# Performance work log

Hardware: AMD Instinct MI355X
Metric: run time of the kernel (lower is better)

The kernel has to match this reference:

```python
import math
import jax, jax.numpy as jnp
import numpy as np

PHI = (1.0 + math.sqrt(5.0)) / 2.0
LUT_SIZE = 4096
_angles = np.arange(LUT_SIZE, dtype=np.float64) * (2.0 * math.pi / LUT_SIZE)
SIN_TABLE = jnp.asarray(np.sin(_angles), dtype=jnp.float32)
COS_TABLE = jnp.asarray(np.cos(_angles), dtype=jnp.float32)


def lut_sin_cos(theta):
    # LUT lookup with linear interpolation over a 4096-entry table on [0, 2pi)
    pos = theta * (LUT_SIZE / (2.0 * math.pi))
    i0f = jnp.floor(pos)
    frac = pos - i0f
    i0 = jnp.mod(i0f.astype(jnp.int32), LUT_SIZE)
    i1 = jnp.mod(i0 + 1, LUT_SIZE)
    sin_v = SIN_TABLE[i0] * (1.0 - frac) + SIN_TABLE[i1] * frac
    cos_v = COS_TABLE[i0] * (1.0 - frac) + COS_TABLE[i1] * frac
    return sin_v, cos_v


def setup_inputs() -> dict:
    key = jax.random.key(0)
    ks = jax.random.split(key, 8)
    B, D = 32768, 1024
    return {
        "x_real": jax.random.normal(ks[0], (B, D), jnp.float32),
        "x_imag": jax.random.normal(ks[1], (B, D), jnp.float32),
        "t": jax.random.uniform(ks[2], (B,), jnp.float32),
        "memory_real": jax.random.normal(ks[3], (B, D), jnp.float32),
        "memory_imag": jax.random.normal(ks[4], (B, D), jnp.float32),
        "w_query": jax.random.normal(ks[5], (D,), jnp.float32) * 0.02,
        "b_query": jnp.zeros((D,), jnp.float32),
        "w_osc": jax.random.normal(ks[6], (D,), jnp.float32) * 0.02,
        "b_osc": jnp.zeros((D,), jnp.float32),
    }


def reference(x_real, x_imag, t, memory_real, memory_imag, w_query, b_query, w_osc, b_osc):
    d_model = x_real.shape[-1]
    scale = math.sqrt(d_model)
    k = 1.0

    t_phi = t[:, None] * PHI                       # [B, 1]

    # query oscillator
    wl_query = 1.0 + jnp.abs(w_query)
    theta_query = x_real / wl_query + b_query      # [B, D]
    sin_q, cos_q = lut_sin_cos(theta_query)
    query_real, query_imag = cos_q, sin_q

    # memory interference (memory is detached state)
    mem_r = jax.lax.stop_gradient(memory_real)
    mem_i = jax.lax.stop_gradient(memory_imag)
    interference_real = jnp.sum(query_real * mem_r + query_imag * mem_i, axis=-1)
    interference_imag = jnp.sum(query_real * mem_i - query_imag * mem_r, axis=-1)
    interference_mag = jnp.sqrt(interference_real ** 2 + interference_imag ** 2)

    # alpha (exponential mode)
    interference_norm = jax.nn.sigmoid(interference_mag / scale - 2.0)
    x_inv = 1.0 - interference_norm
    alpha = jnp.exp(-k * x_inv)
    alpha_exp = alpha[:, None]

    # blend with memory
    blended_real = alpha_exp * x_real + (1.0 - alpha_exp) * mem_r
    blended_imag = alpha_exp * x_imag + (1.0 - alpha_exp) * mem_i

    # evolve oscillator
    wl_osc = 1.0 + jnp.abs(w_osc)
    theta_osc_real = blended_real / wl_osc + b_osc + t_phi
    theta_osc_imag = blended_imag / wl_osc + b_osc + t_phi
    sin_or, cos_or = lut_sin_cos(theta_osc_real)
    sin_oi, cos_oi = lut_sin_cos(theta_osc_imag)
    evolved_real = cos_or * cos_oi - sin_or * sin_oi
    evolved_imag = cos_or * sin_oi + sin_or * cos_oi

    return evolved_real, evolved_imag, alpha
```

## Files before the change

### kernel.cpp

```cpp
#include <hip/hip_runtime.h>
#include <math.h>

static constexpr float PHI_F = 1.61803398874989484820f;

union F4 { float4 v; float f[4]; };

__global__ __launch_bounds__(256) void liquid_echo_kernel(
    const float* __restrict__ x_real,
    const float* __restrict__ x_imag,
    const float* __restrict__ t,
    const float* __restrict__ mem_r,
    const float* __restrict__ mem_i,
    const float* __restrict__ w_query,
    const float* __restrict__ b_query,
    const float* __restrict__ w_osc,
    const float* __restrict__ b_osc,
    float* __restrict__ out_real,
    float* __restrict__ out_imag,
    float* __restrict__ out_alpha,
    int D)
{
    const int row = blockIdx.x;
    const int tid = threadIdx.x;
    const int d0  = tid << 2;
    const size_t base = (size_t)row * (size_t)D + (size_t)d0;

    F4 xr, xi, mr, mi, wq, bq, wo, bo;
    xr.v = *(const float4*)(x_real + base);
    xi.v = *(const float4*)(x_imag + base);
    mr.v = *(const float4*)(mem_r + base);
    mi.v = *(const float4*)(mem_i + base);
    wq.v = *(const float4*)(w_query + d0);
    bq.v = *(const float4*)(b_query + d0);
    wo.v = *(const float4*)(w_osc + d0);
    bo.v = *(const float4*)(b_osc + d0);

    float accr = 0.f, acci = 0.f;
#pragma unroll
    for (int j = 0; j < 4; ++j) {
        float inv = __builtin_amdgcn_rcpf(1.0f + fabsf(wq.f[j]));
        float th  = fmaf(xr.f[j], inv, bq.f[j]);
        float s, c;
        __sincosf(th, &s, &c);
        accr = fmaf(c, mr.f[j], fmaf(s, mi.f[j], accr));
        acci = fmaf(c, mi.f[j], fmaf(-s, mr.f[j], acci));
    }

#pragma unroll
    for (int off = 32; off > 0; off >>= 1) {
        accr += __shfl_down(accr, off, 64);
        acci += __shfl_down(acci, off, 64);
    }
    __shared__ float sred[8];
    const int wave = tid >> 6;
    const int lane = tid & 63;
    if (lane == 0) { sred[wave] = accr; sred[wave + 4] = acci; }
    __syncthreads();
    const float ir = (sred[0] + sred[1]) + (sred[2] + sred[3]);
    const float ii = (sred[4] + sred[5]) + (sred[6] + sred[7]);

    const float mag   = sqrtf(fmaf(ir, ir, ii * ii));
    const float z     = fmaf(mag, 1.0f / 32.0f, -2.0f);
    const float norm  = __builtin_amdgcn_rcpf(1.0f + __expf(-z));
    const float alpha = __expf(norm - 1.0f);
    const float beta  = 1.0f - alpha;
    const float tphi2 = 2.0f * PHI_F * t[row];

    F4 er, ei;
#pragma unroll
    for (int j = 0; j < 4; ++j) {
        float br  = fmaf(alpha, xr.f[j], beta * mr.f[j]);
        float bi  = fmaf(alpha, xi.f[j], beta * mi.f[j]);
        float inv = __builtin_amdgcn_rcpf(1.0f + fabsf(wo.f[j]));
        float ths = fmaf(br + bi, inv, fmaf(2.0f, bo.f[j], tphi2));
        float s, c;
        __sincosf(ths, &s, &c);
        er.f[j] = c;
        ei.f[j] = s;
    }
    *(float4*)(out_real + base) = er.v;
    *(float4*)(out_imag + base) = ei.v;
    if (tid == 0) out_alpha[row] = alpha;
}

extern "C" void kernel_launch(void* const* d_in, const int* in_sizes, int n_in,
                              void* d_out, int out_size, void* d_ws, size_t ws_size,
                              hipStream_t stream) {
    const float* x_real = (const float*)d_in[0];
    const float* x_imag = (const float*)d_in[1];
    const float* t      = (const float*)d_in[2];
    const float* mem_r  = (const float*)d_in[3];
    const float* mem_i  = (const float*)d_in[4];
    const float* w_q    = (const float*)d_in[5];
    const float* b_q    = (const float*)d_in[6];
    const float* w_o    = (const float*)d_in[7];
    const float* b_o    = (const float*)d_in[8];

    const int B = in_sizes[2];
    const int D = in_sizes[5];

    float* out       = (float*)d_out;
    float* out_real  = out;
    float* out_imag  = out + (size_t)B * (size_t)D;
    float* out_alpha = out + 2ull * (size_t)B * (size_t)D;

    liquid_echo_kernel<<<B, 256, 0, stream>>>(
        x_real, x_imag, t, mem_r, mem_i, w_q, b_q, w_o, b_o,
        out_real, out_imag, out_alpha, D);
}
```

Measured before the change: 147.4 us.

## Map one row per wavefront to remove cross-wave shared-memory reduction

Each 64-lane wavefront now processes a whole 1024-element row, with each lane handling 16 elements, so the dot-product reduction is done purely with xor shuffles and no LDS or block barrier. The grid shrinks by four and the weight loads are split, with the oscillator weights loaded after the first phase. This trades the synchronisation cost for much higher register pressure per thread, which may reduce occupancy. It also hardcodes D=1024.

```diff
diff --git a/kernel.cpp b/kernel.cpp
--- a/kernel.cpp
+++ b/kernel.cpp
@@ -5,7 +5,7 @@
 
 union F4 { float4 v; float f[4]; };
 
-__global__ __launch_bounds__(256) void liquid_echo_kernel(
+__global__ __launch_bounds__(256, 4) void liquid_echo_kernel(
     const float* __restrict__ x_real,
     const float* __restrict__ x_imag,
     const float* __restrict__ t,
@@ -17,70 +17,87 @@
     const float* __restrict__ b_osc,
     float* __restrict__ out_real,
     float* __restrict__ out_imag,
-    float* __restrict__ out_alpha,
-    int D)
+    float* __restrict__ out_alpha)
 {
-    const int row = blockIdx.x;
-    const int tid = threadIdx.x;
-    const int d0  = tid << 2;
-    const size_t base = (size_t)row * (size_t)D + (size_t)d0;
+    const int lane = threadIdx.x & 63;
+    const int wave = threadIdx.x >> 6;
+    const int row  = (blockIdx.x << 2) + wave;
+    const size_t rbase = (size_t)row << 10;
 
-    F4 xr, xi, mr, mi, wq, bq, wo, bo;
-    xr.v = *(const float4*)(x_real + base);
-    xi.v = *(const float4*)(x_imag + base);
-    mr.v = *(const float4*)(mem_r + base);
-    mi.v = *(const float4*)(mem_i + base);
-    wq.v = *(const float4*)(w_query + d0);
-    bq.v = *(const float4*)(b_query + d0);
-    wo.v = *(const float4*)(w_osc + d0);
-    bo.v = *(const float4*)(b_osc + d0);
+    const float trow = t[row];
+
+    F4 xr[4], xi[4], mr[4], mi[4];
+#pragma unroll
+    for (int j = 0; j < 4; ++j) {
+        const size_t off = rbase + (size_t)(((j << 6) + lane) << 2);
+        xr[j].v = *(const float4*)(x_real + off);
+        xi[j].v = *(const float4*)(x_imag + off);
+        mr[j].v = *(const float4*)(mem_r + off);
+        mi[j].v = *(const float4*)(mem_i + off);
+    }
+    F4 wq[4], bq[4];
+#pragma unroll
+    for (int j = 0; j < 4; ++j) {
+        const int woff = ((j << 6) + lane) << 2;
+        wq[j].v = *(const float4*)(w_query + woff);
+        bq[j].v = *(const float4*)(b_query + woff);
+    }
 
     float accr = 0.f, acci = 0.f;
 #pragma unroll
     for (int j = 0; j < 4; ++j) {
-        float inv = __builtin_amdgcn_rcpf(1.0f + fabsf(wq.f[j]));
-        float th  = fmaf(xr.f[j], inv, bq.f[j]);
-        float s, c;
-        __sincosf(th, &s, &c);
-        accr = fmaf(c, mr.f[j], fmaf(s, mi.f[j], accr));
-        acci = fmaf(c, mi.f[j], fmaf(-s, mr.f[j], acci));
+#pragma unroll
+        for (int k = 0; k < 4; ++k) {
+            float inv = __builtin_amdgcn_rcpf(1.0f + fabsf(wq[j].f[k]));
+            float th  = fmaf(xr[j].f[k], inv, bq[j].f[k]);
+            float s, c;
+            __sincosf(th, &s, &c);
+            accr = fmaf(c, mr[j].f[k], fmaf(s, mi[j].f[k], accr));
+            acci = fmaf(c, mi[j].f[k], fmaf(-s, mr[j].f[k], acci));
+        }
+    }
+
+    F4 wo[4], bo[4];
+#pragma unroll
+    for (int j = 0; j < 4; ++j) {
+        const int woff = ((j << 6) + lane) << 2;
+        wo[j].v = *(const float4*)(w_osc + woff);
+        bo[j].v = *(const float4*)(b_osc + woff);
     }
 
 #pragma unroll
     for (int off = 32; off > 0; off >>= 1) {
-        accr += __shfl_down(accr, off, 64);
-        acci += __shfl_down(acci, off, 64);
+        accr += __shfl_xor(accr, off, 64);
+        acci += __shfl_xor(acci, off, 64);
     }
-    __shared__ float sred[8];
-    const int wave = tid >> 6;
-    const int lane = tid & 63;
-    if (lane == 0) { sred[wave] = accr; sred[wave + 4] = acci; }
-    __syncthreads();
-    const float ir = (sred[0] + sred[1]) + (sred[2] + sred[3]);
-    const float ii = (sred[4] + sred[5]) + (sred[6] + sred[7]);
 
-    const float mag   = sqrtf(fmaf(ir, ir, ii * ii));
+    const float mag   = sqrtf(fmaf(accr, accr, acci * acci));
     const float z     = fmaf(mag, 1.0f / 32.0f, -2.0f);
     const float norm  = __builtin_amdgcn_rcpf(1.0f + __expf(-z));
     const float alpha = __expf(norm - 1.0f);
     const float beta  = 1.0f - alpha;
-    const float tphi2 = 2.0f * PHI_F * t[row];
+    const float tphi2 = 2.0f * PHI_F * trow;
 
-    F4 er, ei;
 #pragma unroll
     for (int j = 0; j < 4; ++j) {
-        float br  = fmaf(alpha, xr.f[j], beta * mr.f[j]);
-        float bi  = fmaf(alpha, xi.f[j], beta * mi.f[j]);
-        float inv = __builtin_amdgcn_rcpf(1.0f + fabsf(wo.f[j]));
-        float ths = fmaf(br + bi, inv, fmaf(2.0f, bo.f[j], tphi2));
-        float s, c;
-        __sincosf(ths, &s, &c);
-        er.f[j] = c;
-        ei.f[j] = s;
+        F4 er, ei;
+#pragma unroll
+        for (int k = 0; k < 4; ++k) {
+            float br  = fmaf(alpha, xr[j].f[k], beta * mr[j].f[k]);
+            float bi  = fmaf(alpha, xi[j].f[k], beta * mi[j].f[k]);
+            float inv = __builtin_amdgcn_rcpf(1.0f + fabsf(wo[j].f[k]));
+            float ths = fmaf(br + bi, inv, fmaf(2.0f, bo[j].f[k], tphi2));
+            float s, c;
+            __sincosf(ths, &s, &c);
+            er.f[k] = c;
+            ei.f[k] = s;
+        }
+        const size_t off = rbase + (size_t)(((j << 6) + lane) << 2);
+        *(float4*)(out_real + off) = er.v;
+        *(float4*)(out_imag + off) = ei.v;
     }
-    *(float4*)(out_real + base) = er.v;
-    *(float4*)(out_imag + base) = ei.v;
-    if (tid == 0) out_alpha[row] = alpha;
+
+    if (lane == 0) out_alpha[row] = alpha;
 }
 
 extern "C" void kernel_launch(void* const* d_in, const int* in_sizes, int n_in,
@@ -104,7 +121,7 @@
     float* out_imag  = out + (size_t)B * (size_t)D;
     float* out_alpha = out + 2ull * (size_t)B * (size_t)D;
 
-    liquid_echo_kernel<<<B, 256, 0, stream>>>(
+    liquid_echo_kernel<<<B / 4, 256, 0, stream>>>(
         x_real, x_imag, t, mem_r, mem_i, w_q, b_q, w_o, b_o,
-        out_real, out_imag, out_alpha, D);
+        out_real, out_imag, out_alpha);
 }
```

Result: no change. 149.2 us (+1.2%).
